# Performance work log

Hardware: AMD Instinct MI355X
Metric: run time of the kernel (lower is better)

Reference implementation:

```python
import jax, jax.numpy as jnp
import numpy as np

B, M, D, DE = 2, 256, 256, 64  # batch, tokens, in_dim, dep_embed_dim


def setup_inputs() -> dict:
    key = jax.random.key(0)
    ks = jax.random.split(key, 10)
    features = jax.random.normal(ks[0], (B, M + 1, D), jnp.float32)
    dep_type_adj = jax.random.normal(ks[1], (B, M, M, DE), jnp.float32)
    adj = (jax.random.uniform(ks[2], (B, M, M)) < 0.05).astype(jnp.int32)
    idx = jnp.arange(M)
    adj = adj.at[:, idx, idx].set(1)
    asp_start = jax.random.randint(ks[3], (B,), 0, 200, dtype=jnp.int32)
    asp_end = asp_start + 16
    s = lambda fan_in: 1.0 / np.sqrt(fan_in)
    Wz = jax.random.normal(ks[4], (D, D), jnp.float32) * s(D)
    bz = jax.random.normal(ks[5], (D,), jnp.float32) * s(D)
    Wa = jax.random.normal(ks[6], (D + DE + D,), jnp.float32) * s(D + DE + D)
    Wm = jax.random.normal(ks[7], (D, D + DE), jnp.float32) * s(D + DE)
    Wh = jax.random.normal(ks[8], (D, 2 * D), jnp.float32) * s(2 * D)
    return dict(features=features, dep_type_adj=dep_type_adj, deprel_adj=adj,
                asp_start=asp_start, asp_end=asp_end,
                Wz=Wz, bz=bz, Wa=Wa, Wm=Wm, Wh=Wh)


def reference(features, dep_type_adj, deprel_adj, asp_start, asp_end, Wz, bz, Wa, Wm, Wh):
    # z_linear
    zf = features @ Wz.T + bz                              # [B, M+1, D]
    f = zf[:, 1:]                                          # token feats [B, M, D]
    asp = zf[0, 1:]                                        # NOTE: original indexes features[0] (batch 0)

    # candidate neighbors for node i: out-edges (i,j) then in-edges (j,i) -> 2M slots
    dep_cat = jnp.concatenate([dep_type_adj, jnp.swapaxes(dep_type_adj, 1, 2)], axis=2)  # [B,M,2M,DE]
    mask = jnp.concatenate([deprel_adj, jnp.swapaxes(deprel_adj, 1, 2)], axis=2) != 0    # [B,M,2M]

    # attention_layer weight split over [dep | neighbor_feat | aspect_feat]
    wa_dep, wa_nf, wa_asp = Wa[:DE], Wa[DE:DE + D], Wa[DE + D:]
    s = (jnp.einsum('bike,e->bik', dep_cat, wa_dep)
         + jnp.tile(f @ wa_nf, (1, 2))[:, None, :]
         + (asp @ wa_asp)[None, :, None])                  # [B,M,2M]
    s = jnp.where(s > 0, s, 0.01 * s)                      # LeakyReLU(0.01)
    big_neg = jnp.finfo(s.dtype).min
    w = jax.nn.softmax(jnp.where(mask, s, big_neg), axis=-1)
    w = jnp.where(mask, w, 0.0)                            # edge-softmax over valid neighbors

    # w_m over [dep | neighbor_feat]
    Wm_dep, Wm_f = Wm[:, :DE], Wm[:, DE:]
    nf_proj = jnp.tile(f @ Wm_f.T, (1, 2, 1))              # [B,2M,D], neighbor part (i-independent)
    msg = jax.nn.relu(jnp.einsum('bike,de->bikd', dep_cat, Wm_dep) + nf_proj[:, None])  # [B,M,2M,D]
    fused = jnp.einsum('bik,bikd->bid', w, msg)            # weighted aggregate [B,M,D]

    # w_h over [fused | aspect]
    out_asp = jax.nn.relu(fused @ Wh[:, :D].T + (asp @ Wh[:, D:].T)[None])  # [B,M,D]

    # only aspect-span nodes are updated; +1 offset into the token axis
    pos = jnp.arange(M)
    upd = (pos[None, :] >= asp_start[:, None]) & (pos[None, :] < asp_end[:, None])  # [B,M]
    tokens = jnp.where(upd[..., None], out_asp, features[:, 1:])
    return jnp.concatenate([features[:, :1], tokens], axis=1)  # dropout is identity at inference
```

## Files before the change

kernel.cpp:

```cpp
#include <hip/hip_runtime.h>
#include <hip/hip_bf16.h>
#include <cstdint>

#define BB 2
#define MM 256
#define DD 256
#define DE 64
#define K2 (2*MM)
#define WM_LD (DD+DE)
#define WH_LD (2*DD)
#define DEP_LD 68

__device__ float g_fz    [MM*DD];
__device__ float g_fproj [BB*MM*DD];
__device__ float g_fnf   [BB*MM];
__device__ float g_aspdot[MM];
__device__ float g_asph  [MM*DD];
__device__ float g_WzT   [DD*DD];
__device__ float g_WmT   [DD*DD];
__device__ float g_WmDepT[DE*DD];
__device__ float g_WhT   [2*DD*DD];

__global__ __launch_bounds__(256) void k_tr(const float* __restrict__ Wz,
                                            const float* __restrict__ Wm,
                                            const float* __restrict__ Wh,
                                            const float4* __restrict__ src,
                                            float4* __restrict__ dst, int n4) {
  const int t = threadIdx.x;
  const int blk = blockIdx.x;
  if (blk < 256) {
    const int d = blk;
    g_WzT[t*DD + d] = Wz[(size_t)d*DD + t];
  } else if (blk < 512) {
    const int d = blk - 256;
    g_WmT[t*DD + d] = Wm[(size_t)d*WM_LD + DE + t];
    if (t < DE) g_WmDepT[t*DD + d] = Wm[(size_t)d*WM_LD + t];
  } else {
    const int idx = blk - 512;
    const int d = idx & 255, half = idx >> 8;
    g_WhT[(size_t)(half*DD + t)*DD + d] = Wh[(size_t)d*WH_LD + half*DD + t];
  }
  const int gidx = blk*256 + t;
  if (gidx < n4) dst[gidx] = src[gidx];
}

__global__ __launch_bounds__(256) void k_pre(const float* __restrict__ feats,
                                             const float* __restrict__ bz,
                                             const float* __restrict__ Wa) {
  const int blk = blockIdx.x;
  const int b   = blk >> 7;
  const int m0  = (blk & 127) * 2;
  const int t   = threadIdx.x;

  __shared__ float fin[2][DD];
  __shared__ float fzsh[2][DD];

  fin[0][t] = feats[((size_t)b*(MM+1) + m0 + 1)*DD + t];
  fin[1][t] = feats[((size_t)b*(MM+1) + m0 + 2)*DD + t];
  __syncthreads();

  float a0 = 0.f, a1 = 0.f;
  #pragma unroll 8
  for (int e4 = 0; e4 < DD/4; ++e4) {
    const float4 f0 = *(const float4*)&fin[0][e4*4];
    const float4 f1 = *(const float4*)&fin[1][e4*4];
    const float w0 = g_WzT[(e4*4+0)*DD + t];
    const float w1 = g_WzT[(e4*4+1)*DD + t];
    const float w2 = g_WzT[(e4*4+2)*DD + t];
    const float w3 = g_WzT[(e4*4+3)*DD + t];
    a0 += f0.x*w0 + f0.y*w1 + f0.z*w2 + f0.w*w3;
    a1 += f1.x*w0 + f1.y*w1 + f1.z*w2 + f1.w*w3;
  }
  const float bzt = bz[t];
  a0 += bzt; a1 += bzt;
  fzsh[0][t] = a0; fzsh[1][t] = a1;
  if (b == 0) {
    g_fz[(size_t)(m0    )*DD + t] = a0;
    g_fz[(size_t)(m0 + 1)*DD + t] = a1;
  }
  __syncthreads();

  const int wv = t >> 6, lane = t & 63;
  if (wv < 2) {
    float p = 0.f;
    for (int e = lane; e < DD; e += 64) p += fzsh[wv][e] * Wa[DE + e];
    for (int off = 32; off > 0; off >>= 1) p += __shfl_down(p, off, 64);
    if (lane == 0) g_fnf[b*MM + m0 + wv] = p;
  } else if (b == 0) {
    const int rr = wv - 2;
    float p = 0.f;
    for (int e = lane; e < DD; e += 64) p += fzsh[rr][e] * Wa[DE + DD + e];
    for (int off = 32; off > 0; off >>= 1) p += __shfl_down(p, off, 64);
    if (lane == 0) g_aspdot[m0 + rr] = p;
  }

  float p0 = 0.f, p1 = 0.f;
  #pragma unroll 8
  for (int e4 = 0; e4 < DD/4; ++e4) {
    const float4 f0 = *(const float4*)&fzsh[0][e4*4];
    const float4 f1 = *(const float4*)&fzsh[1][e4*4];
    const float w0 = g_WmT[(e4*4+0)*DD + t];
    const float w1 = g_WmT[(e4*4+1)*DD + t];
    const float w2 = g_WmT[(e4*4+2)*DD + t];
    const float w3 = g_WmT[(e4*4+3)*DD + t];
    p0 += f0.x*w0 + f0.y*w1 + f0.z*w2 + f0.w*w3;
    p1 += f1.x*w0 + f1.y*w1 + f1.z*w2 + f1.w*w3;
  }
  g_fproj[((size_t)b*MM + m0    )*DD + t] = p0;
  g_fproj[((size_t)b*MM + m0 + 1)*DD + t] = p1;

  if (b == 0) {
    float q0 = 0.f, q1 = 0.f;
    #pragma unroll 8
    for (int e4 = 0; e4 < DD/4; ++e4) {
      const float4 f0 = *(const float4*)&fzsh[0][e4*4];
      const float4 f1 = *(const float4*)&fzsh[1][e4*4];
      const float w0 = g_WhT[(size_t)(DD + e4*4+0)*DD + t];
      const float w1 = g_WhT[(size_t)(DD + e4*4+1)*DD + t];
      const float w2 = g_WhT[(size_t)(DD + e4*4+2)*DD + t];
      const float w3 = g_WhT[(size_t)(DD + e4*4+3)*DD + t];
      q0 += f0.x*w0 + f0.y*w1 + f0.z*w2 + f0.w*w3;
      q1 += f1.x*w0 + f1.y*w1 + f1.z*w2 + f1.w*w3;
    }
    g_asph[(size_t)(m0    )*DD + t] = q0;
    g_asph[(size_t)(m0 + 1)*DD + t] = q1;
  }
}

__global__ __launch_bounds__(256, 1) void k_attn(const float* __restrict__ dta,
                                                 const int*   __restrict__ adj,
                                                 const int*   __restrict__ a_start,
                                                 const int*   __restrict__ a_end,
                                                 const float* __restrict__ Wa,
                                                 float* __restrict__ out) {
  const int b = blockIdx.x >> 4;
  const int r = blockIdx.x & 15;
  const int i = a_start[b] + r;
  if (i >= a_end[b] || i >= MM) return;
  const int t = threadIdx.x;
  const int lane = t & 63, wv = t >> 6;
  const int d = t;

  __shared__ int   act[K2];
  __shared__ float sv [K2];
  __shared__ int   wcnt[8];
  __shared__ float wrm [4];
  __shared__ float wrs [4];
  __shared__ float wadep[DE];
  __shared__ float fnfsh[MM];
  __shared__ float depsh[64*DEP_LD];
  __shared__ float fused_sh[DD];

  const int mval0 = adj[((size_t)b*MM + i)*MM + t];
  const int mval1 = adj[((size_t)b*MM + t)*MM + i];
  float wm[DE];
  #pragma unroll
  for (int e = 0; e < DE; ++e) wm[e] = g_WmDepT[e*DD + d];
  fnfsh[t] = g_fnf[b*MM + t];
  if (t < DE) wadep[t] = Wa[t];
  const float aspdot_i = g_aspdot[i];
  const float asph_i   = g_asph[(size_t)i*DD + d];

  const bool on0 = (mval0 != 0);
  const bool on1 = (mval1 != 0);
  const unsigned long long b0 = __ballot(on0);
  const unsigned long long b1 = __ballot(on1);
  if (lane == 0) { wcnt[wv] = __popcll(b0); wcnt[4+wv] = __popcll(b1); }
  __syncthreads();
  const int tot0 = wcnt[0] + wcnt[1] + wcnt[2] + wcnt[3];
  const int na   = tot0 + wcnt[4] + wcnt[5] + wcnt[6] + wcnt[7];
  {
    int off0 = 0, off1 = tot0;
    for (int w2 = 0; w2 < wv; ++w2) { off0 += wcnt[w2]; off1 += wcnt[4+w2]; }
    off0 += __popcll(b0 & ((1ull << lane) - 1ull));
    off1 += __popcll(b1 & ((1ull << lane) - 1ull));
    if (on0) act[off0] = t;
    if (on1) act[off1] = MM + t;
  }
  __syncthreads();

  const int jj = t >> 2, sub = t & 3;
  for (int base = 0; base < na; base += 64) {
    const int j = base + jj;
    float p = 0.f; int k = 0;
    if (j < na) {
      k = act[j];
      const float* dv = (k < MM) ? dta + (((size_t)b*MM + i)*MM + k)*DE
                                 : dta + (((size_t)b*MM + (k - MM))*MM + i)*DE;
      const float4* dv4 = (const float4*)dv + sub*4;
      const float4 v0 = dv4[0], v1 = dv4[1], v2 = dv4[2], v3 = dv4[3];
      const float* wa = wadep + sub*16;
      p = v0.x*wa[0]  + v0.y*wa[1]  + v0.z*wa[2]  + v0.w*wa[3]
        + v1.x*wa[4]  + v1.y*wa[5]  + v1.z*wa[6]  + v1.w*wa[7]
        + v2.x*wa[8]  + v2.y*wa[9]  + v2.z*wa[10] + v2.w*wa[11]
        + v3.x*wa[12] + v3.y*wa[13] + v3.z*wa[14] + v3.w*wa[15];
      if (base == 0) {
        float4* ds = (float4*)(depsh + jj*DEP_LD + sub*16);
        ds[0] = v0; ds[1] = v1; ds[2] = v2; ds[3] = v3;
      }
    }
    p += __shfl_xor(p, 1, 64);
    p += __shfl_xor(p, 2, 64);
    if (j < na && sub == 0) {
      const float s = p + fnfsh[k & (MM-1)] + aspdot_i;
      sv[j] = (s > 0.f) ? s : 0.01f * s;
    }
  }
  __syncthreads();

  {
    float part = -3.4e38f;
    for (int j = t; j < na; j += 256) part = fmaxf(part, sv[j]);
    for (int off = 32; off > 0; off >>= 1) part = fmaxf(part, __shfl_down(part, off, 64));
    if (lane == 0) wrm[wv] = part;
  }
  __syncthreads();
  const float mx = fmaxf(fmaxf(wrm[0], wrm[1]), fmaxf(wrm[2], wrm[3]));
  {
    float psum = 0.f;
    for (int j = t; j < na; j += 256) { float e = expf(sv[j] - mx); sv[j] = e; psum += e; }
    for (int off = 32; off > 0; off >>= 1) psum += __shfl_down(psum, off, 64);
    if (lane == 0) wrs[wv] = psum;
  }
  __syncthreads();
  const float inv = 1.f / (wrs[0] + wrs[1] + wrs[2] + wrs[3]);
  for (int j = t; j < na; j += 256) sv[j] *= inv;
  __syncthreads();

  float acc = 0.f;
  for (int base = 0; base < na; base += 64) {
    const int cnt = min(64, na - base);
    if (base > 0) {
      __syncthreads();
      const int nf4 = cnt * (DE/4);
      for (int q = t; q < nf4; q += 256) {
        const int jl = q >> 4, e4 = q & 15;
        const int k = act[base + jl];
        const float* dv = (k < MM) ? dta + (((size_t)b*MM + i)*MM + k)*DE
                                   : dta + (((size_t)b*MM + (k - MM))*MM + i)*DE;
        *(float4*)(depsh + jl*DEP_LD + e4*4) = ((const float4*)dv)[e4];
      }
      __syncthreads();
    }
    #pragma unroll 2
    for (int jl = 0; jl < cnt; ++jl) {
      const int k = act[base + jl];
      const float* dp = depsh + jl*DEP_LD;
      float dot = 0.f;
      #pragma unroll
      for (int e4 = 0; e4 < DE/4; ++e4) {
        const float4 v = *(const float4*)(dp + 4*e4);
        dot += v.x*wm[4*e4] + v.y*wm[4*e4+1] + v.z*wm[4*e4+2] + v.w*wm[4*e4+3];
      }
      float msg = dot + g_fproj[((size_t)b*MM + (k & (MM-1)))*DD + d];
      msg = (msg > 0.f) ? msg : 0.f;
      acc += sv[base + jl] * msg;
    }
  }
  fused_sh[d] = acc;
  __syncthreads();

  float o = asph_i;
  #pragma unroll 8
  for (int e4 = 0; e4 < DD/4; ++e4) {
    const float f0 = fused_sh[4*e4+0], f1 = fused_sh[4*e4+1];
    const float f2 = fused_sh[4*e4+2], f3 = fused_sh[4*e4+3];
    o += f0 * g_WhT[(size_t)(4*e4+0)*DD + d]
       + f1 * g_WhT[(size_t)(4*e4+1)*DD + d]
       + f2 * g_WhT[(size_t)(4*e4+2)*DD + d]
       + f3 * g_WhT[(size_t)(4*e4+3)*DD + d];
  }
  out[((size_t)b*(MM+1) + i + 1)*DD + d] = (o > 0.f) ? o : 0.f;
}

extern "C" void kernel_launch(void* const* d_in, const int* in_sizes, int n_in,
                              void* d_out, int out_size, void* d_ws, size_t ws_size,
                              hipStream_t stream) {
  const float* feats   = (const float*)d_in[0];
  const float* dta     = (const float*)d_in[1];
  const int*   adj     = (const int*)  d_in[2];
  const int*   a_start = (const int*)  d_in[3];
  const int*   a_end   = (const int*)  d_in[4];
  const float* Wz      = (const float*)d_in[5];
  const float* bz      = (const float*)d_in[6];
  const float* Wa      = (const float*)d_in[7];
  const float* Wm      = (const float*)d_in[8];
  const float* Wh      = (const float*)d_in[9];
  float* out = (float*)d_out;

  const int n4 = BB*(MM+1)*DD/4;
  k_tr  <<<1024, 256, 0, stream>>>(Wz, Wm, Wh, (const float4*)feats, (float4*)out, n4);
  k_pre <<<BB*MM/2, 256, 0, stream>>>(feats, bz, Wa);
  k_attn<<<BB*16, 256, 0, stream>>>(dta, adj, a_start, a_end, Wa, out);
}
```

Before: 147.9 us.

## Tile weight transposes via LDS into float4-packed layouts and stage fproj in shared memory

The weight transpose kernel now uses a 64x65 LDS tile per block and writes float4-interleaved weight layouts, so 132 blocks replace 1024 strided-write blocks. The GEMV loops in the pre and attention kernels read one float4 per step instead of four scalar loads. The attention kernel also gathers the neighbor fproj rows into a 64KB shared buffer, prefetched into registers during the softmax. This trades register pressure and large LDS usage for coalesced, reused loads, and drops the unused g_fz store.

```diff
diff --git a/kernel.cpp b/kernel.cpp
--- a/kernel.cpp
+++ b/kernel.cpp
@@ -11,37 +11,45 @@
 #define WH_LD (2*DD)
 #define DEP_LD 68
 
-__device__ float g_fz    [MM*DD];
+__device__ float4 g_Wz4   [64*DD];
+__device__ float4 g_Wm4   [64*DD];
+__device__ float4 g_WmDep4[16*DD];
+__device__ float4 g_Wh4lo [64*DD];
+__device__ float4 g_Wh4hi [64*DD];
 __device__ float g_fproj [BB*MM*DD];
 __device__ float g_fnf   [BB*MM];
 __device__ float g_aspdot[MM];
 __device__ float g_asph  [MM*DD];
-__device__ float g_WzT   [DD*DD];
-__device__ float g_WmT   [DD*DD];
-__device__ float g_WmDepT[DE*DD];
-__device__ float g_WhT   [2*DD*DD];
 
 __global__ __launch_bounds__(256) void k_tr(const float* __restrict__ Wz,
                                             const float* __restrict__ Wm,
                                             const float* __restrict__ Wh,
                                             const float4* __restrict__ src,
                                             float4* __restrict__ dst, int n4) {
-  const int t = threadIdx.x;
-  const int blk = blockIdx.x;
-  if (blk < 256) {
-    const int d = blk;
-    g_WzT[t*DD + d] = Wz[(size_t)d*DD + t];
-  } else if (blk < 512) {
-    const int d = blk - 256;
-    g_WmT[t*DD + d] = Wm[(size_t)d*WM_LD + DE + t];
-    if (t < DE) g_WmDepT[t*DD + d] = Wm[(size_t)d*WM_LD + t];
-  } else {
-    const int idx = blk - 512;
-    const int d = idx & 255, half = idx >> 8;
-    g_WhT[(size_t)(half*DD + t)*DD + d] = Wh[(size_t)d*WH_LD + half*DD + t];
-  }
+  const int t = threadIdx.x, blk = blockIdx.x;
+  const int c = t & 63, r0 = t >> 6;
+  __shared__ float tile[64][65];
+
   const int gidx = blk*256 + t;
   if (gidx < n4) dst[gidx] = src[gidx];
+
+  const float* s = nullptr; float4* d4 = nullptr;
+  int ld = 0, row0 = 0, col0 = 0, e4base = 0;
+  if (blk < 16)      { s = Wz; ld = DD;    row0 = (blk>>2)*64; col0 = (blk&3)*64;      d4 = g_Wz4;    e4base = (blk&3)*16; }
+  else if (blk < 32) { int x = blk-16; s = Wm; ld = WM_LD; row0 = (x>>2)*64; col0 = DE + (x&3)*64; d4 = g_Wm4; e4base = (x&3)*16; }
+  else if (blk < 36) { int x = blk-32; s = Wm; ld = WM_LD; row0 = x*64;      col0 = 0;             d4 = g_WmDep4; e4base = 0; }
+  else if (blk < 68) { int x = blk-36; int rt = x>>3, cg = x&7; s = Wh; ld = WH_LD; row0 = rt*64; col0 = cg*64;
+                       d4 = (cg < 4) ? g_Wh4lo : g_Wh4hi; e4base = (cg&3)*16; }
+  if (s) {
+    #pragma unroll
+    for (int rr = r0; rr < 64; rr += 4)
+      tile[rr][c] = s[(size_t)(row0 + rr)*ld + col0 + c];
+    __syncthreads();
+    #pragma unroll
+    for (int je = r0; je < 16; je += 4)
+      d4[(size_t)(e4base + je)*DD + row0 + c] =
+        make_float4(tile[c][4*je+0], tile[c][4*je+1], tile[c][4*je+2], tile[c][4*je+3]);
+  }
 }
 
 __global__ __launch_bounds__(256) void k_pre(const float* __restrict__ feats,
@@ -61,23 +69,16 @@
 
   float a0 = 0.f, a1 = 0.f;
   #pragma unroll 8
-  for (int e4 = 0; e4 < DD/4; ++e4) {
+  for (int e4 = 0; e4 < 64; ++e4) {
+    const float4 w  = g_Wz4[(size_t)e4*DD + t];
     const float4 f0 = *(const float4*)&fin[0][e4*4];
     const float4 f1 = *(const float4*)&fin[1][e4*4];
-    const float w0 = g_WzT[(e4*4+0)*DD + t];
-    const float w1 = g_WzT[(e4*4+1)*DD + t];
-    const float w2 = g_WzT[(e4*4+2)*DD + t];
-    const float w3 = g_WzT[(e4*4+3)*DD + t];
-    a0 += f0.x*w0 + f0.y*w1 + f0.z*w2 + f0.w*w3;
-    a1 += f1.x*w0 + f1.y*w1 + f1.z*w2 + f1.w*w3;
+    a0 += f0.x*w.x + f0.y*w.y + f0.z*w.z + f0.w*w.w;
+    a1 += f1.x*w.x + f1.y*w.y + f1.z*w.z + f1.w*w.w;
   }
   const float bzt = bz[t];
   a0 += bzt; a1 += bzt;
   fzsh[0][t] = a0; fzsh[1][t] = a1;
-  if (b == 0) {
-    g_fz[(size_t)(m0    )*DD + t] = a0;
-    g_fz[(size_t)(m0 + 1)*DD + t] = a1;
-  }
   __syncthreads();
 
   const int wv = t >> 6, lane = t & 63;
@@ -96,15 +97,12 @@
 
   float p0 = 0.f, p1 = 0.f;
   #pragma unroll 8
-  for (int e4 = 0; e4 < DD/4; ++e4) {
+  for (int e4 = 0; e4 < 64; ++e4) {
+    const float4 w  = g_Wm4[(size_t)e4*DD + t];
     const float4 f0 = *(const float4*)&fzsh[0][e4*4];
     const float4 f1 = *(const float4*)&fzsh[1][e4*4];
-    const float w0 = g_WmT[(e4*4+0)*DD + t];
-    const float w1 = g_WmT[(e4*4+1)*DD + t];
-    const float w2 = g_WmT[(e4*4+2)*DD + t];
-    const float w3 = g_WmT[(e4*4+3)*DD + t];
-    p0 += f0.x*w0 + f0.y*w1 + f0.z*w2 + f0.w*w3;
-    p1 += f1.x*w0 + f1.y*w1 + f1.z*w2 + f1.w*w3;
+    p0 += f0.x*w.x + f0.y*w.y + f0.z*w.z + f0.w*w.w;
+    p1 += f1.x*w.x + f1.y*w.y + f1.z*w.z + f1.w*w.w;
   }
   g_fproj[((size_t)b*MM + m0    )*DD + t] = p0;
   g_fproj[((size_t)b*MM + m0 + 1)*DD + t] = p1;
@@ -112,15 +110,12 @@
   if (b == 0) {
     float q0 = 0.f, q1 = 0.f;
     #pragma unroll 8
-    for (int e4 = 0; e4 < DD/4; ++e4) {
+    for (int e4 = 0; e4 < 64; ++e4) {
+      const float4 w  = g_Wh4hi[(size_t)e4*DD + t];
       const float4 f0 = *(const float4*)&fzsh[0][e4*4];
       const float4 f1 = *(const float4*)&fzsh[1][e4*4];
-      const float w0 = g_WhT[(size_t)(DD + e4*4+0)*DD + t];
-      const float w1 = g_WhT[(size_t)(DD + e4*4+1)*DD + t];
-      const float w2 = g_WhT[(size_t)(DD + e4*4+2)*DD + t];
-      const float w3 = g_WhT[(size_t)(DD + e4*4+3)*DD + t];
-      q0 += f0.x*w0 + f0.y*w1 + f0.z*w2 + f0.w*w3;
-      q1 += f1.x*w0 + f1.y*w1 + f1.z*w2 + f1.w*w3;
+      q0 += f0.x*w.x + f0.y*w.y + f0.z*w.z + f0.w*w.w;
+      q1 += f1.x*w.x + f1.y*w.y + f1.z*w.z + f1.w*w.w;
     }
     g_asph[(size_t)(m0    )*DD + t] = q0;
     g_asph[(size_t)(m0 + 1)*DD + t] = q1;
@@ -149,13 +144,14 @@
   __shared__ float wadep[DE];
   __shared__ float fnfsh[MM];
   __shared__ float depsh[64*DEP_LD];
+  __shared__ float fproj_sh[64][DD];
   __shared__ float fused_sh[DD];
 
   const int mval0 = adj[((size_t)b*MM + i)*MM + t];
   const int mval1 = adj[((size_t)b*MM + t)*MM + i];
-  float wm[DE];
+  float4 wm4[16];
   #pragma unroll
-  for (int e = 0; e < DE; ++e) wm[e] = g_WmDepT[e*DD + d];
+  for (int e4 = 0; e4 < 16; ++e4) wm4[e4] = g_WmDep4[(size_t)e4*DD + d];
   fnfsh[t] = g_fnf[b*MM + t];
   if (t < DE) wadep[t] = Wa[t];
   const float aspdot_i = g_aspdot[i];
@@ -206,6 +202,19 @@
       sv[j] = (s > 0.f) ? s : 0.01f * s;
     }
   }
+
+  const int cnt0 = (na < 64) ? na : 64;
+  const int nq0  = cnt0 * 64;
+  float4 stash[16];
+  #pragma unroll
+  for (int rr = 0; rr < 16; ++rr) {
+    const int q = t + rr*256;
+    if (q < nq0) {
+      const int jl = q >> 6, c4 = q & 63;
+      const int k = act[jl];
+      stash[rr] = *((const float4*)(g_fproj + ((size_t)b*MM + (k & (MM-1)))*DD) + c4);
+    }
+  }
   __syncthreads();
 
   {
@@ -225,6 +234,11 @@
   __syncthreads();
   const float inv = 1.f / (wrs[0] + wrs[1] + wrs[2] + wrs[3]);
   for (int j = t; j < na; j += 256) sv[j] *= inv;
+  #pragma unroll
+  for (int rr = 0; rr < 16; ++rr) {
+    const int q = t + rr*256;
+    if (q < nq0) { const int jl = q >> 6, c4 = q & 63; *(float4*)&fproj_sh[jl][c4*4] = stash[rr]; }
+  }
   __syncthreads();
 
   float acc = 0.f;
@@ -232,8 +246,13 @@
     const int cnt = min(64, na - base);
     if (base > 0) {
       __syncthreads();
-      const int nf4 = cnt * (DE/4);
-      for (int q = t; q < nf4; q += 256) {
+      for (int q = t; q < cnt*64; q += 256) {
+        const int jl = q >> 6, c4 = q & 63;
+        const int k = act[base + jl];
+        *(float4*)&fproj_sh[jl][c4*4] =
+          *((const float4*)(g_fproj + ((size_t)b*MM + (k & (MM-1)))*DD) + c4);
+      }
+      for (int q = t; q < cnt*16; q += 256) {
         const int jl = q >> 4, e4 = q & 15;
         const int k = act[base + jl];
         const float* dv = (k < MM) ? dta + (((size_t)b*MM + i)*MM + k)*DE
@@ -244,15 +263,15 @@
     }
     #pragma unroll 2
     for (int jl = 0; jl < cnt; ++jl) {
-      const int k = act[base + jl];
-      const float* dp = depsh + jl*DEP_LD;
+      const float4* dp = (const float4*)(depsh + jl*DEP_LD);
       float dot = 0.f;
       #pragma unroll
-      for (int e4 = 0; e4 < DE/4; ++e4) {
-        const float4 v = *(const float4*)(dp + 4*e4);
-        dot += v.x*wm[4*e4] + v.y*wm[4*e4+1] + v.z*wm[4*e4+2] + v.w*wm[4*e4+3];
+      for (int e4 = 0; e4 < 16; ++e4) {
+        const float4 v = dp[e4];
+        const float4 w = wm4[e4];
+        dot += v.x*w.x + v.y*w.y + v.z*w.z + v.w*w.w;
       }
-      float msg = dot + g_fproj[((size_t)b*MM + (k & (MM-1)))*DD + d];
+      float msg = dot + fproj_sh[jl][d];
       msg = (msg > 0.f) ? msg : 0.f;
       acc += sv[base + jl] * msg;
     }
@@ -262,13 +281,10 @@
 
   float o = asph_i;
   #pragma unroll 8
-  for (int e4 = 0; e4 < DD/4; ++e4) {
-    const float f0 = fused_sh[4*e4+0], f1 = fused_sh[4*e4+1];
-    const float f2 = fused_sh[4*e4+2], f3 = fused_sh[4*e4+3];
-    o += f0 * g_WhT[(size_t)(4*e4+0)*DD + d]
-       + f1 * g_WhT[(size_t)(4*e4+1)*DD + d]
-       + f2 * g_WhT[(size_t)(4*e4+2)*DD + d]
-       + f3 * g_WhT[(size_t)(4*e4+3)*DD + d];
+  for (int e4 = 0; e4 < 64; ++e4) {
+    const float4 w = g_Wh4lo[(size_t)e4*DD + d];
+    const float4 f = *(const float4*)&fused_sh[e4*4];
+    o += f.x*w.x + f.y*w.y + f.z*w.z + f.w*w.w;
   }
   out[((size_t)b*(MM+1) + i + 1)*DD + d] = (o > 0.f) ? o : 0.f;
 }
@@ -289,7 +305,7 @@
   float* out = (float*)d_out;
 
   const int n4 = BB*(MM+1)*DD/4;
-  k_tr  <<<1024, 256, 0, stream>>>(Wz, Wm, Wh, (const float4*)feats, (float4*)out, n4);
+  k_tr  <<<132, 256, 0, stream>>>(Wz, Wm, Wh, (const float4*)feats, (float4*)out, n4);
   k_pre <<<BB*MM/2, 256, 0, stream>>>(feats, bz, Wa);
   k_attn<<<BB*16, 256, 0, stream>>>(dta, adj, a_start, a_end, Wa, out);
 }
```

Result: faster. 144.1 us (-2.5%).
